# Kernel optimization log

Measured on AMD Instinct MI355X. Metric: run time of the kernel, lower is better.

Reference implementation:

```python
import jax, jax.numpy as jnp
import numpy as np
import math

STRIDE = ((2, 2), (4, 4), (8, 8), (16, 16))  # (ws, hs) pairs
D_MODEL = 256
B, H, W = 8, 128, 128
BN_EPS = 1e-5
LEAKY_SLOPE = 0.2


def setup_inputs() -> dict:
    key = jax.random.key(0)
    ks = jax.random.split(key, 8)
    s = 1.0 / math.sqrt(D_MODEL)
    s3 = 1.0 / math.sqrt(D_MODEL * 9)
    return {
        "x": jax.random.normal(ks[0], (B, D_MODEL, H, W), jnp.float32),
        "wq": jax.random.normal(ks[1], (D_MODEL, D_MODEL, 1, 1), jnp.float32) * s,
        "bq": jnp.zeros((D_MODEL,), jnp.float32),
        "wk": jax.random.normal(ks[2], (D_MODEL, D_MODEL, 1, 1), jnp.float32) * s,
        "bk": jnp.zeros((D_MODEL,), jnp.float32),
        "wv": jax.random.normal(ks[3], (D_MODEL, D_MODEL, 1, 1), jnp.float32) * s,
        "bv": jnp.zeros((D_MODEL,), jnp.float32),
        "wo": jax.random.normal(ks[4], (D_MODEL, D_MODEL, 3, 3), jnp.float32) * s3,
        "bo": jnp.zeros((D_MODEL,), jnp.float32),
        "gamma": jnp.ones((D_MODEL,), jnp.float32),
        "beta": jnp.zeros((D_MODEL,), jnp.float32),
    }


def _conv1x1(x, w, bias):
    # 1x1 conv == channel matmul
    return jnp.einsum('bchw,oc->bohw', x, w[:, :, 0, 0]) + bias[None, :, None, None]


def reference(x, wq, bq, wk, bk, wv, bv, wo, bo, gamma, beta):
    b, c, h, w = x.shape
    n = len(STRIDE)
    d_k = c // n
    q = _conv1x1(x, wq, bq)
    k = _conv1x1(x, wk, bk)
    v = _conv1x1(x, wv, bv)
    outs = []
    for idx, (ws, hs) in enumerate(STRIDE):
        lo = idx * d_k
        oh, ow = h // hs, w // ws

        def gather(t):
            # strided patch gather: element (i,j) head <- t[:, :, i::hs, j::ws]
            t = t[:, lo:lo + d_k].reshape(b, d_k, oh, hs, ow, ws)
            return t.transpose(0, 3, 5, 1, 2, 4).reshape(b, hs * ws, d_k * oh * ow)

        qi, ki, vi = gather(q), gather(k), gather(v)
        scale = 1.0 / jnp.sqrt(jnp.asarray(qi.shape[-1], qi.dtype))
        scores = jnp.einsum('bsd,btd->bst', qi, ki) * scale  # [b, hs*ws, hs*ws]
        p = jax.nn.softmax(scores, axis=-1)
        y = jnp.einsum('bst,btd->bsd', p, vi)
        # scatter back exactly as the torch permute(0,3,1,4,2,5): h = i*oh + row
        y = y.reshape(b, hs, ws, d_k, oh, ow).transpose(0, 3, 1, 4, 2, 5).reshape(b, d_k, h, w)
        outs.append(y)
    out = jnp.concatenate(outs, axis=1)  # [b, c, h, w]
    # output_linear: 3x3 conv -> BatchNorm2d (training-mode batch stats) -> LeakyReLU(0.2)
    out = jax.lax.conv_general_dilated(out, wo, (1, 1), 'SAME',
                                       dimension_numbers=('NCHW', 'OIHW', 'NCHW'))
    out = out + bo[None, :, None, None]
    mean = out.mean(axis=(0, 2, 3))
    var = out.var(axis=(0, 2, 3))
    out = (out - mean[None, :, None, None]) * jax.lax.rsqrt(var[None, :, None, None] + BN_EPS)
    out = out * gamma[None, :, None, None] + beta[None, :, None, None]
    return jnp.where(out > 0, out, LEAKY_SLOPE * out)
```

## Files before the change

kernel.cpp:

```cpp
#include <hip/hip_runtime.h>
#include <stdint.h>


#define DEVI static __device__ __forceinline__

typedef short bf8 __attribute__((ext_vector_type(8)));
typedef float f32x4 __attribute__((ext_vector_type(4)));

DEVI unsigned short f2bf(float f) {
  unsigned u = __builtin_bit_cast(unsigned, f);
  u = (u + 0x7fffu + ((u >> 16) & 1u)) >> 16;
  return (unsigned short)u;
}
DEVI float bf2f(unsigned short h) {
  unsigned u = ((unsigned)h) << 16;
  return __builtin_bit_cast(float, u);
}

DEVI void gload16(const void* g, void* l) {
  __builtin_amdgcn_global_load_lds(
      (const __attribute__((address_space(1))) unsigned int*)g,
      (__attribute__((address_space(3))) unsigned int*)l, 16, 0, 0);
}

static const size_t WB_OFF  = 0;
static const size_t WOB_OFF = 393216;
static const size_t QN_OFF  = 1572864;
static const size_t KN_OFF  = QN_OFF + 67108864;
static const size_t VN_OFF  = KN_OFF + 67108864;
static const size_t YN_OFF  = VN_OFF + 67108864;
static const size_t SC_OFF  = YN_OFF + 67108864;
static const size_t PRB_OFF = SC_OFF + 2236928;
static const size_t BNP_OFF = PRB_OFF + 1118464;
static const size_t BNS_OFF = BNP_OFF + 4194304;
static const size_t ZP_OFF  = BNS_OFF + 2048;
static const size_t WS_NEED = ZP_OFF + 256;

__global__ void k_prep(const float* __restrict__ wq, const float* __restrict__ wk,
                       const float* __restrict__ wv, const float* __restrict__ wo,
                       unsigned short* __restrict__ Wb, unsigned short* __restrict__ Wob) {
  int i = blockIdx.x * 256 + threadIdx.x;
  if (i < 196608) {
    int z = i >> 16, r = i & 65535;
    const float* w = (z == 0) ? wq : (z == 1) ? wk : wv;
    Wb[i] = f2bf(w[r]);
  } else {
    int j = i - 196608;
    int o = j / 2304, k = j - o * 2304;
    int e = k >> 8, c = k & 255;
    Wob[j] = f2bf(wo[(o * 256 + c) * 9 + e]);
  }
}

__global__ void k_zero(float* __restrict__ p, int n) {
  int i = blockIdx.x * 256 + threadIdx.x;
  for (; i < n; i += gridDim.x * 256) p[i] = 0.f;
}

__global__ __launch_bounds__(256, 3) void k_qkv(
    const float* __restrict__ x, const unsigned short* __restrict__ Wb,
    const float* __restrict__ bq, const float* __restrict__ bk, const float* __restrict__ bv,
    unsigned short* __restrict__ Qn, unsigned short* __restrict__ Kn,
    unsigned short* __restrict__ Vn) {
  const int pt = blockIdx.x, b = blockIdx.y;
  const int p0 = pt * 64;
  const int tid = threadIdx.x;

  __shared__ __align__(16) unsigned short xt[64 * 256];
  __shared__ __align__(16) unsigned short ot[32 * 256];

  const float* xb = x + (size_t)b * 256 * 16384;
  for (int k = 0; k < 16; ++k) {
    int i = tid + k * 256;
    int c = i >> 4, p4 = (i & 15) * 4;
    float4 v = *(const float4*)(xb + (size_t)c * 16384 + p0 + p4);
    xt[(p4 + 0) * 256 + (c ^ (((p4 + 0) & 7) << 3))] = f2bf(v.x);
    xt[(p4 + 1) * 256 + (c ^ (((p4 + 1) & 7) << 3))] = f2bf(v.y);
    xt[(p4 + 2) * 256 + (c ^ (((p4 + 2) & 7) << 3))] = f2bf(v.z);
    xt[(p4 + 3) * 256 + (c ^ (((p4 + 3) & 7) << 3))] = f2bf(v.w);
  }
  __syncthreads();

  const int wave = tid >> 6, lane = tid & 63;
  const int lr = lane & 15, lk = lane >> 4;
  const int obase = wave * 64;

  for (int z = 0; z < 3; ++z) {
    const unsigned short* Wz = Wb + (size_t)z * 65536;
    f32x4 acc[4][4];
    for (int m = 0; m < 4; ++m)
      for (int n = 0; n < 4; ++n)
        for (int r = 0; r < 4; ++r) acc[m][n][r] = 0.f;

    for (int ks = 0; ks < 8; ++ks) {
      int c0 = ks * 32 + lk * 8;
      bf8 a[4], bb[4];
#pragma unroll
      for (int m = 0; m < 4; ++m)
        a[m] = *(const bf8*)(Wz + (size_t)(obase + m * 16 + lr) * 256 + c0);
#pragma unroll
      for (int n = 0; n < 4; ++n) {
        int p = n * 16 + lr;
        bb[n] = *(const bf8*)(&xt[p * 256 + (c0 ^ ((p & 7) << 3))]);
      }
#pragma unroll
      for (int m = 0; m < 4; ++m)
#pragma unroll
        for (int n = 0; n < 4; ++n)
          acc[m][n] = __builtin_amdgcn_mfma_f32_16x16x32_bf16(a[m], bb[n], acc[m][n], 0, 0, 0);
    }

    const float* bias = (z == 0) ? bq : (z == 1) ? bk : bv;
    unsigned short* On = (z == 0) ? Qn : (z == 1) ? Kn : Vn;
    for (int h = 0; h < 2; ++h) {
      __syncthreads();
#pragma unroll
      for (int m = 0; m < 4; ++m) {
        int ob4 = obase + m * 16 + lk * 4;
        float4 b4 = *(const float4*)(bias + ob4);
#pragma unroll
        for (int nn = 0; nn < 2; ++nn) {
          int n = h * 2 + nn;
          int pch = nn * 16 + lr;
          ushort4 v4;
          v4.x = f2bf(acc[m][n][0] + b4.x);
          v4.y = f2bf(acc[m][n][1] + b4.y);
          v4.z = f2bf(acc[m][n][2] + b4.z);
          v4.w = f2bf(acc[m][n][3] + b4.w);
          *(ushort4*)(&ot[pch * 256 + (ob4 ^ ((pch & 7) << 3))]) = v4;
        }
      }
      __syncthreads();
      unsigned short* gb = On + ((size_t)b * 16384 + p0 + h * 32) * 256;
#pragma unroll
      for (int i = 0; i < 4; ++i) {
        int ch = tid + i * 256;
        *(uint4*)(gb + ch * 8) = *(const uint4*)(&ot[ch * 8]);
      }
    }
  }
}

template <int IDX>
__global__ __launch_bounds__(256) void k_gram(
    const unsigned short* __restrict__ Qn, const unsigned short* __restrict__ Kn,
    float* __restrict__ scores) {
  constexpr int HS = 2 << IDX, S = HS * HS, OH = 64 >> IDX, NSP = OH * OH;
  constexpr int SPW = (IDX == 2) ? 2 : 8;
  constexpr int DSUB = SPW * 64;
  constexpr int SPB = NSP / 32;
  constexpr int STEPS = SPB / SPW;
  constexpr int ROWS = S;
  constexpr int TPT = S * SPW * 8 / 256;
  constexpr int SCOFF = (IDX == 0) ? 0 : (IDX == 1) ? 128 : 2176;
  constexpr int HC = IDX * 64;
  constexpr int MT = (IDX == 2) ? 4 : 1;

  const int chk = blockIdx.x, b = blockIdx.y;
  const int tid = threadIdx.x;
  const int wave = tid >> 6, lane = tid & 63, lr = lane & 15, lk = lane >> 4;

  __shared__ __align__(16) unsigned short qg[ROWS * DSUB];
  __shared__ __align__(16) unsigned short kg[ROWS * DSUB];
  __shared__ float red[S * S];

  const size_t base = (size_t)b * 16384 * 256;

  f32x4 acc[MT][MT];
  for (int m = 0; m < MT; ++m)
    for (int n = 0; n < MT; ++n)
      for (int r = 0; r < 4; ++r) acc[m][n][r] = 0.f;

  for (int st = 0; st < STEPS; ++st) {
    const int sp0 = chk * SPB + st * SPW;
    __syncthreads();
#pragma unroll
    for (int r = 0; r < TPT; ++r) {
      int task = tid + r * 256;
      int cg = task & 7, pl = task >> 3;
      int spl = pl >> (2 * (IDX + 1)), s = pl & (S - 1);
      int sp = sp0 + spl;
      int ohi = sp >> (6 - IDX), owi = sp & (OH - 1);
      int ii = s >> (IDX + 1), jj = s & (HS - 1);
      int p = (ohi * HS + ii) * 128 + owi * HS + jj;
      size_t gaddr = base + (size_t)p * 256 + HC + ((cg ^ (p & 7)) << 3);
      int laddr = s * DSUB + (((spl * 8 + cg) ^ (s & 7)) << 3);
      *(uint4*)(qg + laddr) = *(const uint4*)(Qn + gaddr);
      *(uint4*)(kg + laddr) = *(const uint4*)(Kn + gaddr);
    }
    __syncthreads();
    if (IDX == 2) {
      int kgid = wave * 4 + lk;
      bf8 a[4], bb[4];
#pragma unroll
      for (int m = 0; m < 4; ++m) {
        int row = m * 16 + lr;
        int off = row * DSUB + ((kgid ^ (row & 7)) << 3);
        a[m] = *(const bf8*)(qg + off);
        bb[m] = *(const bf8*)(kg + off);
      }
#pragma unroll
      for (int m = 0; m < 4; ++m)
#pragma unroll
        for (int n = 0; n < 4; ++n)
          acc[m][n] = __builtin_amdgcn_mfma_f32_16x16x32_bf16(a[m], bb[n], acc[m][n], 0, 0, 0);
    } else {
      int row = lr & (ROWS - 1);
#pragma unroll
      for (int kk = 0; kk < 4; ++kk) {
        int kgid = (wave * 4 + kk) * 4 + lk;
        int off = row * DSUB + ((kgid ^ (row & 7)) << 3);
        bf8 a = *(const bf8*)(qg + off);
        bf8 bb = *(const bf8*)(kg + off);
        acc[0][0] = __builtin_amdgcn_mfma_f32_16x16x32_bf16(a, bb, acc[0][0], 0, 0, 0);
      }
    }
  }

  __syncthreads();
  for (int i2 = tid; i2 < S * S; i2 += 256) red[i2] = 0.f;
  __syncthreads();
  if (IDX == 2) {
#pragma unroll
    for (int m = 0; m < 4; ++m)
#pragma unroll
      for (int n = 0; n < 4; ++n)
#pragma unroll
        for (int r = 0; r < 4; ++r)
          atomicAdd(&red[(m * 16 + lk * 4 + r) * 64 + n * 16 + lr], acc[m][n][r]);
  } else if (IDX == 1) {
#pragma unroll
    for (int r = 0; r < 4; ++r)
      atomicAdd(&red[(lk * 4 + r) * 16 + lr], acc[0][0][r]);
  } else {
    if (lk == 0 && lr < 4) {
#pragma unroll
      for (int r = 0; r < 4; ++r)
        atomicAdd(&red[r * 4 + lr], acc[0][0][r]);
    }
  }
  __syncthreads();
  float* sc = scores + SCOFF + (size_t)b * S * S;
  for (int i2 = tid; i2 < S * S; i2 += 256) atomicAdd(sc + i2, red[i2]);
}

__global__ __launch_bounds__(256) void k_gram3(
    const unsigned short* __restrict__ Qn, const unsigned short* __restrict__ Kn,
    float* __restrict__ part3) {
  const int qc = blockIdx.x, tq = blockIdx.y, b = blockIdx.z;
  const int tid = threadIdx.x;
  const int wave = tid >> 6, lane = tid & 63, lr = lane & 15, lk = lane >> 4;

  __shared__ __align__(16) unsigned short qg[256 * 64];
  __shared__ __align__(16) unsigned short kg[64 * 64];

  const size_t base = (size_t)b * 16384 * 256;

  f32x4 acc[4][4];
  for (int m = 0; m < 4; ++m)
    for (int n = 0; n < 4; ++n)
      for (int r = 0; r < 4; ++r) acc[m][n][r] = 0.f;

  for (int st = 0; st < 8; ++st) {
    int sp = qc * 8 + st;
    int ohi = sp >> 3, owi = sp & 7;
    __syncthreads();
#pragma unroll
    for (int r = 0; r < 8; ++r) {
      int task = tid + r * 256;
      int cg = task & 7, s = task >> 3;
      int p = (ohi * 16 + (s >> 4)) * 128 + owi * 16 + (s & 15);
      uint4 v = *(const uint4*)(Qn + base + (size_t)p * 256 + 192 + ((cg ^ (p & 7)) << 3));
      *(uint4*)(qg + s * 64 + ((cg ^ (s & 7)) << 3)) = v;
    }
#pragma unroll
    for (int r = 0; r < 2; ++r) {
      int task = tid + r * 256;
      int cg = task & 7, tl = task >> 3;
      int p = (ohi * 16 + tq * 4 + (tl >> 4)) * 128 + owi * 16 + (tl & 15);
      uint4 v = *(const uint4*)(Kn + base + (size_t)p * 256 + 192 + ((cg ^ (p & 7)) << 3));
      *(uint4*)(kg + tl * 64 + ((cg ^ (tl & 7)) << 3)) = v;
    }
    __syncthreads();
#pragma unroll
    for (int kk = 0; kk < 2; ++kk) {
      int kgid = kk * 4 + lk;
      bf8 a[4], bb[4];
#pragma unroll
      for (int m = 0; m < 4; ++m) {
        int row = wave * 64 + m * 16 + lr;
        a[m] = *(const bf8*)(qg + row * 64 + ((kgid ^ (row & 7)) << 3));
      }
#pragma unroll
      for (int n = 0; n < 4; ++n) {
        int rowb = n * 16 + lr;
        bb[n] = *(const bf8*)(kg + rowb * 64 + ((kgid ^ (rowb & 7)) << 3));
      }
#pragma unroll
      for (int m = 0; m < 4; ++m)
#pragma unroll
        for (int n = 0; n < 4; ++n)
          acc[m][n] = __builtin_amdgcn_mfma_f32_16x16x32_bf16(a[m], bb[n], acc[m][n], 0, 0, 0);
    }
  }

  float* pb = part3 + (((size_t)qc * 8 + b) * 65536);
#pragma unroll
  for (int m = 0; m < 4; ++m)
#pragma unroll
    for (int r = 0; r < 4; ++r) {
      int srow = wave * 64 + m * 16 + lk * 4 + r;
#pragma unroll
      for (int n = 0; n < 4; ++n)
        pb[srow * 256 + tq * 64 + n * 16 + lr] = acc[m][n][r];
    }
}

__global__ __launch_bounds__(256) void k_softmax(const float* __restrict__ scores,
                                                 unsigned short* __restrict__ prb) {
  const int idx = blockIdx.x, b = blockIdx.y;
  const int S = 4 << (2 * idx);
  const int off = (idx == 0 ? 0 : idx == 1 ? 128 : 2176) + b * S * S;
  const int s = threadIdx.x;
  if (s >= S) return;
  const float scale = rsqrtf(64.0f * (float)(4096 >> (2 * idx)));
  const float* row = scores + off + s * S;
  float m = -1e30f;
  for (int t = 0; t < S; ++t) m = fmaxf(m, row[t]);
  m *= scale;
  float sum = 0.f;
  for (int t = 0; t < S; ++t) sum += __expf(row[t] * scale - m);
  float inv = 1.0f / sum;
  unsigned short* prow = prb + off + s * S;
  for (int t = 0; t < S; ++t) prow[t] = f2bf(__expf(row[t] * scale - m) * inv);
}

__global__ __launch_bounds__(256) void k_softmax3(const float* __restrict__ part3,
                                                  unsigned short* __restrict__ prb) {
  const int sc_ = blockIdx.x, b = blockIdx.y;
  const int tid = threadIdx.x;
  const int s = sc_ * 32 + (tid >> 3);
  const int t0 = (tid & 7) * 32;
  float v[32];
#pragma unroll
  for (int k = 0; k < 32; ++k) v[k] = 0.f;
  for (int q = 0; q < 8; ++q) {
    const float4* pp = (const float4*)(part3 + (((size_t)q * 8 + b) * 256 + s) * 256 + t0);
#pragma unroll
    for (int k = 0; k < 8; ++k) {
      float4 u = pp[k];
      v[k * 4 + 0] += u.x; v[k * 4 + 1] += u.y; v[k * 4 + 2] += u.z; v[k * 4 + 3] += u.w;
    }
  }
  const float scale = 1.0f / 64.0f;
  float m = -1e30f;
#pragma unroll
  for (int k = 0; k < 32; ++k) { v[k] *= scale; m = fmaxf(m, v[k]); }
  m = fmaxf(m, __shfl_xor(m, 1));
  m = fmaxf(m, __shfl_xor(m, 2));
  m = fmaxf(m, __shfl_xor(m, 4));
  float sum = 0.f;
#pragma unroll
  for (int k = 0; k < 32; ++k) { v[k] = __expf(v[k] - m); sum += v[k]; }
  sum += __shfl_xor(sum, 1);
  sum += __shfl_xor(sum, 2);
  sum += __shfl_xor(sum, 4);
  float inv = 1.0f / sum;
  unsigned short* prw = prb + 34944 + (size_t)b * 65536 + s * 256 + t0;
#pragma unroll
  for (int k8 = 0; k8 < 4; ++k8) {
    unsigned short tmp[8];
#pragma unroll
    for (int e = 0; e < 8; ++e) tmp[e] = f2bf(v[k8 * 8 + e] * inv);
    *(uint4*)(prw + k8 * 8) = *(const uint4*)tmp;
  }
}

template <int IDX>
__global__ __launch_bounds__(256) void k_pv(
    const unsigned short* __restrict__ Vn, const unsigned short* __restrict__ prb,
    unsigned short* __restrict__ Yn) {
  constexpr int HS = 2 << IDX, S = HS * HS, OH = 64 >> IDX;
  constexpr int IT = (IDX == 0) ? 8 : (IDX == 1) ? 4 : 1;
  constexpr int POFF = (IDX == 0) ? 0 : (IDX == 1) ? 128 : 2176;
  const int bx = blockIdx.x, b = blockIdx.y;
  const int c = threadIdx.x & 63, spg = threadIdx.x >> 6;
  __shared__ __align__(16) float pl[S * S];
  const unsigned short* pr = prb + POFF + (size_t)b * S * S;
  for (int i = threadIdx.x; i < S * S; i += 256) pl[i] = bf2f(pr[i]);
  __syncthreads();
  const int hc = IDX * 64;
  const unsigned short* vb = Vn + (size_t)b * 16384 * 256;
  unsigned short* yb = Yn + (size_t)b * 16384 * 256;
  for (int it = 0; it < IT; ++it) {
    int sp = bx * (4 * IT) + it * 4 + spg;
    int ohi = sp >> (6 - IDX), owi = sp & (OH - 1);
    float v[S];
#pragma unroll
    for (int t = 0; t < S; ++t) {
      int po = (ohi * HS + t / HS) * 128 + owi * HS + (t % HS);
      v[t] = bf2f(vb[(size_t)po * 256 + ((hc + c) ^ ((po & 7) << 3))]);
    }
    for (int s = 0; s < S; ++s) {
      const float4* p4 = (const float4*)(pl + s * S);
      float a = 0.f;
#pragma unroll
      for (int t4 = 0; t4 < S / 4; ++t4) {
        float4 pp = p4[t4];
        a += pp.x * v[t4 * 4] + pp.y * v[t4 * 4 + 1] + pp.z * v[t4 * 4 + 2] + pp.w * v[t4 * 4 + 3];
      }
      int po = ((s >> (IDX + 1)) * OH + ohi) * 128 + (s & (HS - 1)) * OH + owi;
      yb[(size_t)po * 256 + ((hc + c) ^ ((po & 7) << 3))] = f2bf(a);
    }
  }
}

__global__ __launch_bounds__(256) void k_pv3(
    const unsigned short* __restrict__ Vn, const unsigned short* __restrict__ prb,
    unsigned short* __restrict__ Yn) {
  const int sp = blockIdx.x, b = blockIdx.y;
  const int ohi = sp >> 3, owi = sp & 7;
  const int tid = threadIdx.x;
  __shared__ __align__(16) unsigned short vl[64 * 256];
  const unsigned short* vb = Vn + (size_t)b * 16384 * 256;
  {
    int t = tid;
    int po = (ohi * 16 + (t >> 4)) * 128 + owi * 16 + (t & 15);
    const unsigned short* src = vb + (size_t)po * 256;
    int xv = (po & 7) << 3;
#pragma unroll
    for (int g = 0; g < 8; ++g) {
      ushort4 lo = *(const ushort4*)(src + ((192 + g * 8) ^ xv));
      ushort4 hi = *(const ushort4*)(src + ((192 + g * 8) ^ xv) + 4);
      unsigned short vv[8] = {lo.x, lo.y, lo.z, lo.w, hi.x, hi.y, hi.z, hi.w};
#pragma unroll
      for (int e = 0; e < 8; ++e) {
        int cc = g * 8 + e;
        vl[cc * 256 + (t ^ ((cc & 7) << 3))] = vv[e];
      }
    }
  }
  __syncthreads();

  const int wave = tid >> 6, lane = tid & 63;
  const int lr = lane & 15, lk = lane >> 4;
  const int sb = wave * 64;
  const unsigned short* pr = prb + 34944 + (size_t)b * 65536;

  f32x4 acc[4][4];
  for (int m = 0; m < 4; ++m)
    for (int n = 0; n < 4; ++n)
      for (int r = 0; r < 4; ++r) acc[m][n][r] = 0.f;

  for (int kk = 0; kk < 8; ++kk) {
    int t0 = kk * 32 + lk * 8;
    bf8 a[4], bb[4];
#pragma unroll
    for (int m = 0; m < 4; ++m)
      a[m] = *(const bf8*)(pr + (size_t)(sb + m * 16 + lr) * 256 + t0);
#pragma unroll
    for (int n = 0; n < 4; ++n) {
      int cc = n * 16 + lr;
      bb[n] = *(const bf8*)(&vl[cc * 256 + (t0 ^ ((cc & 7) << 3))]);
    }
#pragma unroll
    for (int m = 0; m < 4; ++m)
#pragma unroll
      for (int n = 0; n < 4; ++n)
        acc[m][n] = __builtin_amdgcn_mfma_f32_16x16x32_bf16(a[m], bb[n], acc[m][n], 0, 0, 0);
  }

  unsigned short* yb = Yn + (size_t)b * 16384 * 256;
#pragma unroll
  for (int m = 0; m < 4; ++m) {
#pragma unroll
    for (int r = 0; r < 4; ++r) {
      int s = sb + m * 16 + lk * 4 + r;
      int si = s >> 4, sj = s & 15;
      int po = (si * 8 + ohi) * 128 + sj * 8 + owi;
#pragma unroll
      for (int n = 0; n < 4; ++n) {
        int cc = 192 + n * 16 + lr;
        yb[(size_t)po * 256 + (cc ^ (owi << 3))] = f2bf(acc[m][n][r]);
      }
    }
  }
}

#define CONV_PHASE(KT_, R_, PK_, DOSTAGE_, WAITMODE_)                            \
  do {                                                                           \
    if (DOSTAGE_) {                                                              \
      constexpr int type_ = (R_ == 0) ? 0 : (R_ == 1) ? 2 : (R_ == 2) ? 3 : 1;   \
      STAGE((1 - (PK_)) * 4 + (R_), type_, (KT_) + 1);                           \
    }                                                                            \
    if ((WAITMODE_) == 0) { asm volatile("s_waitcnt vmcnt(6)" ::: "memory"); }   \
    else if ((WAITMODE_) == 1) { asm volatile("s_waitcnt vmcnt(0)" ::: "memory"); } \
    __builtin_amdgcn_s_barrier();                                                \
    asm volatile("" ::: "memory");                                               \
    {                                                                            \
      constexpr int mh_ = (R_) >> 1, nh_ = (R_) & 1;                             \
      constexpr int sA_ = (PK_) * 4 + (mh_ ? 3 : 0);                             \
      constexpr int sB_ = (PK_) * 4 + (nh_ ? 2 : 1);                             \
      if (nh_ == 0) {                                                            \
        _Pragma("unroll") for (int m2 = 0; m2 < 4; ++m2) {                       \
          int row = wm * 64 + m2 * 16 + lr;                                      \
          _Pragma("unroll") for (int kk = 0; kk < 2; ++kk)                       \
            areg[m2][kk] = *(const bf8*)(&lds[sA_][row * 64 +                    \
                (((kk * 4 + lk) ^ (row & 7)) << 3)]);                            \
        }                                                                        \
      }                                                                          \
      bf8 breg[2][2];                                                            \
      _Pragma("unroll") for (int n2 = 0; n2 < 2; ++n2) {                         \
        int row = wn * 32 + n2 * 16 + lr;                                        \
        _Pragma("unroll") for (int kk = 0; kk < 2; ++kk)                         \
          breg[n2][kk] = *(const bf8*)(&lds[sB_][row * 64 +                      \
              (((kk * 4 + lk) ^ (row & 7)) << 3)]);                              \
      }                                                                          \
      __builtin_amdgcn_s_setprio(1);                                             \
      _Pragma("unroll") for (int kk = 0; kk < 2; ++kk)                           \
        _Pragma("unroll") for (int m2 = 0; m2 < 4; ++m2)                         \
          _Pragma("unroll") for (int n2 = 0; n2 < 2; ++n2)                       \
            acc[mh_ * 4 + m2][nh_ * 2 + n2] =                                    \
                __builtin_amdgcn_mfma_f32_16x16x32_bf16(                         \
                    areg[m2][kk], breg[n2][kk],                                  \
                    acc[mh_ * 4 + m2][nh_ * 2 + n2], 0, 0, 0);                   \
      __builtin_amdgcn_s_setprio(0);                                             \
      asm volatile("" ::: "memory");                                             \
    }                                                                            \
  } while (0)

__global__ __launch_bounds__(512, 2) void k_conv(
    const unsigned short* __restrict__ Yn, const unsigned short* __restrict__ Wob,
    const float* __restrict__ bo, const unsigned short* __restrict__ zp,
    unsigned short* __restrict__ co, float* __restrict__ bnp) {
  __shared__ __align__(16) unsigned short lds[8][8192];

  const int bid = blockIdx.x;
  const int swz = (bid & 7) * 64 + (bid >> 3);
  const int b = swz >> 6, tile = swz & 63;
  const int y0 = (tile >> 3) * 16, x0 = (tile & 7) * 16;
  const int tid = threadIdx.x;
  const int wave = tid >> 6, lane = tid & 63;
  const int lr = lane & 15, lk = lane >> 4;
  const int wm = wave >> 2, wn = wave & 3;
  const int cg = lane & 7;

  const unsigned short* yb = Yn + (size_t)b * 16384 * 256;

  auto STAGE = [&](int slot, int type, int KT) {
    if (type < 2) {
      const unsigned short* wsrc = Wob + (KT >> 2) * 256 + (KT & 3) * 64;
#pragma unroll
      for (int j = 0; j < 2; ++j) {
        int rp = (wave * 2 + j) * 8 + (lane >> 3);
        int o = ((rp >> 6) & 1) * 128 + type * 64 + (rp & 63);
        int kg = cg ^ (rp & 7);
        gload16(wsrc + o * 2304 + (kg << 3), &lds[slot][(wave * 2 + j) * 512]);
      }
    } else {
      int e = KT >> 2;
      int dy = e / 3 - 1, dx = e % 3 - 1, c8 = (KT & 3) * 8;
#pragma unroll
      for (int j = 0; j < 2; ++j) {
        int rp = (wave * 2 + j) * 8 + (lane >> 3);
        int n = ((rp >> 5) & 3) * 64 + (type - 2) * 32 + (rp & 31);
        int kg = cg ^ (rp & 7);
        int h = y0 + (n >> 4) + dy, ww = x0 + (n & 15) + dx;
        const unsigned short* src = zp;
        if (h >= 0 && h < 128 && ww >= 0 && ww < 128) {
          int pp = h * 128 + ww;
          src = yb + (size_t)pp * 256 + ((c8 + (kg ^ (pp & 7))) << 3);
        }
        gload16(src, &lds[slot][(wave * 2 + j) * 512]);
      }
    }
  };

  f32x4 acc[8][4];
#pragma unroll
  for (int m = 0; m < 8; ++m)
#pragma unroll
    for (int n = 0; n < 4; ++n)
#pragma unroll
      for (int r = 0; r < 4; ++r) acc[m][n][r] = 0.f;

  bf8 areg[4][2];

  STAGE(0, 0, 0); STAGE(1, 2, 0); STAGE(2, 3, 0); STAGE(3, 1, 0);
  asm volatile("s_waitcnt vmcnt(0)" ::: "memory");

  for (int gg = 0; gg < 17; ++gg) {
    const int k0 = gg * 2;
    CONV_PHASE(k0, 0, 0, true, 0);
    CONV_PHASE(k0, 1, 0, true, 0);
    CONV_PHASE(k0, 2, 0, true, 0);
    CONV_PHASE(k0, 3, 0, true, 0);
    CONV_PHASE(k0 + 1, 0, 1, true, 0);
    CONV_PHASE(k0 + 1, 1, 1, true, 0);
    CONV_PHASE(k0 + 1, 2, 1, true, 0);
    CONV_PHASE(k0 + 1, 3, 1, true, 0);
  }
  CONV_PHASE(34, 0, 0, true, 0);
  CONV_PHASE(34, 1, 0, true, 0);
  CONV_PHASE(34, 2, 0, true, 0);
  CONV_PHASE(34, 3, 0, true, 0);
  CONV_PHASE(35, 0, 1, false, 1);
  CONV_PHASE(35, 1, 1, false, 2);
  CONV_PHASE(35, 2, 1, false, 2);
  CONV_PHASE(35, 3, 1, false, 2);

  __syncthreads();
  unsigned short* cb = co + (size_t)b * 256 * 16384;
  float* red1 = (float*)&lds[0][0];
  float* red2 = red1 + 1024;
#pragma unroll
  for (int m = 0; m < 8; ++m) {
#pragma unroll
    for (int r = 0; r < 4; ++r) {
      int o = wm * 128 + m * 16 + lk * 4 + r;
      float bvv = bo[o];
      float s1 = 0.f, s2 = 0.f;
#pragma unroll
      for (int n = 0; n < 4; ++n) {
        int pix = wn * 64 + n * 16 + lr;
        int py = pix >> 4, px = pix & 15;
        float v = acc[m][n][r] + bvv;
        cb[(size_t)o * 16384 + (y0 + py) * 128 + x0 + px] = f2bf(v);
        s1 += v;
        s2 += v * v;
      }
      for (int off = 1; off < 16; off <<= 1) {
        s1 += __shfl_xor(s1, off, 64);
        s2 += __shfl_xor(s2, off, 64);
      }
      if (lr == 0) {
        int ol = m * 16 + lk * 4 + r;
        red1[wave * 128 + ol] = s1;
        red2[wave * 128 + ol] = s2;
      }
    }
  }
  __syncthreads();
  {
    int o = tid & 255, stat = tid >> 8;
    int wm2 = o >> 7, ol = o & 127;
    const float* rd = stat ? red2 : red1;
    float s = rd[(wm2 * 4 + 0) * 128 + ol] + rd[(wm2 * 4 + 1) * 128 + ol] +
              rd[(wm2 * 4 + 2) * 128 + ol] + rd[(wm2 * 4 + 3) * 128 + ol];
    bnp[((size_t)(b * 64 + tile) * 256 + o) * 2 + stat] = s;
  }
}

__global__ __launch_bounds__(256) void k_bnred(
    const float* __restrict__ bnp, const float* __restrict__ gamma,
    const float* __restrict__ beta, float* __restrict__ bns) {
  const int o = blockIdx.x;
  const int tid = threadIdx.x;
  float s1 = 0.f, s2 = 0.f;
  for (int k = tid; k < 512; k += 256) {
    s1 += bnp[((size_t)k * 256 + o) * 2 + 0];
    s2 += bnp[((size_t)k * 256 + o) * 2 + 1];
  }
  __shared__ float r1[256], r2[256];
  r1[tid] = s1; r2[tid] = s2;
  __syncthreads();
  for (int off = 128; off > 0; off >>= 1) {
    if (tid < off) { r1[tid] += r1[tid + off]; r2[tid] += r2[tid + off]; }
    __syncthreads();
  }
  if (tid == 0) {
    const float cnt = 8.0f * 16384.0f;
    float mean = r1[0] / cnt;
    float var = r2[0] / cnt - mean * mean;
    float sc = gamma[o] * rsqrtf(var + 1e-5f);
    bns[o] = sc;
    bns[256 + o] = beta[o] - mean * sc;
  }
}

__global__ void k_bnapply(const unsigned short* __restrict__ co, float* __restrict__ out,
                          const float* __restrict__ bns) {
  size_t i = ((size_t)blockIdx.x * 256 + threadIdx.x) * 8;
  const size_t total = 33554432;
  const size_t stride = (size_t)gridDim.x * 256 * 8;
  for (; i < total; i += stride) {
    uint4 v = *(const uint4*)(co + i);
    int o = (int)((i >> 14) & 255);
    float sc = bns[o], shv = bns[256 + o];
    const unsigned short* pv = (const unsigned short*)&v;
    float r[8];
#pragma unroll
    for (int e = 0; e < 8; ++e) {
      float f = bf2f(pv[e]) * sc + shv;
      r[e] = f > 0.f ? f : 0.2f * f;
    }
    *(float4*)(out + i) = *(const float4*)&r[0];
    *(float4*)(out + i + 4) = *(const float4*)&r[4];
  }
}

extern "C" void kernel_launch(void* const* d_in, const int* in_sizes, int n_in,
                              void* d_out, int out_size, void* d_ws, size_t ws_size,
                              hipStream_t stream) {
  if (ws_size < WS_NEED) return;

  const float* x     = (const float*)d_in[0];
  const float* wq    = (const float*)d_in[1];
  const float* bq    = (const float*)d_in[2];
  const float* wk    = (const float*)d_in[3];
  const float* bk    = (const float*)d_in[4];
  const float* wv    = (const float*)d_in[5];
  const float* bv    = (const float*)d_in[6];
  const float* wo    = (const float*)d_in[7];
  const float* bo    = (const float*)d_in[8];
  const float* gamma = (const float*)d_in[9];
  const float* beta  = (const float*)d_in[10];
  float* out = (float*)d_out;
  char* ws = (char*)d_ws;

  unsigned short* Wb  = (unsigned short*)(ws + WB_OFF);
  unsigned short* Wob = (unsigned short*)(ws + WOB_OFF);
  unsigned short* Qn  = (unsigned short*)(ws + QN_OFF);
  unsigned short* Kn  = (unsigned short*)(ws + KN_OFF);
  unsigned short* Vn  = (unsigned short*)(ws + VN_OFF);
  unsigned short* Yn  = (unsigned short*)(ws + YN_OFF);
  float* part3 = (float*)(ws + YN_OFF);
  unsigned short* co = (unsigned short*)(ws + QN_OFF);
  float* scores = (float*)(ws + SC_OFF);
  unsigned short* prb = (unsigned short*)(ws + PRB_OFF);
  float* bnp    = (float*)(ws + BNP_OFF);
  float* bns    = (float*)(ws + BNS_OFF);
  unsigned short* zp = (unsigned short*)(ws + ZP_OFF);

  k_prep<<<dim3(3072), dim3(256), 0, stream>>>(wq, wk, wv, wo, Wb, Wob);
  k_zero<<<dim3(137), dim3(256), 0, stream>>>(scores, 34944);
  k_zero<<<dim3(1), dim3(64), 0, stream>>>((float*)zp, 64);
  k_qkv<<<dim3(256, 8), dim3(256), 0, stream>>>(x, Wb, bq, bk, bv, Qn, Kn, Vn);
  k_gram<0><<<dim3(32, 8), dim3(256), 0, stream>>>(Qn, Kn, scores);
  k_gram<1><<<dim3(32, 8), dim3(256), 0, stream>>>(Qn, Kn, scores);
  k_gram<2><<<dim3(32, 8), dim3(256), 0, stream>>>(Qn, Kn, scores);
  k_gram3<<<dim3(8, 4, 8), dim3(256), 0, stream>>>(Qn, Kn, part3);
  k_softmax<<<dim3(3, 8), dim3(256), 0, stream>>>(scores, prb);
  k_softmax3<<<dim3(8, 8), dim3(256), 0, stream>>>(part3, prb);
  k_pv<0><<<dim3(128, 8), dim3(256), 0, stream>>>(Vn, prb, Yn);
  k_pv<1><<<dim3(64, 8), dim3(256), 0, stream>>>(Vn, prb, Yn);
  k_pv<2><<<dim3(64, 8), dim3(256), 0, stream>>>(Vn, prb, Yn);
  k_pv3<<<dim3(64, 8), dim3(256), 0, stream>>>(Vn, prb, Yn);
  k_conv<<<dim3(512), dim3(512), 0, stream>>>(Yn, Wob, bo, zp, co, bnp);
  k_bnred<<<dim3(256), dim3(256), 0, stream>>>(bnp, gamma, beta, bns);
  k_bnapply<<<dim3(4096), dim3(256), 0, stream>>>(co, out, bns);
}
```

Before: 572.0 us.

## Hoist conv staging address math, reuse B fragments, merge zero kernels

The 3x3 conv main loop now runs over the 9 kernel taps with quarter-phase unrolling. Per-thread load offsets are precomputed once, so each stage does only cheap adds and one bounds check instead of divides and mods. B-operand fragments are loaded only in the first two phases of each quarter and reused for the second M half, which cuts LDS reads. The two zeroing kernels are merged into one launch, and the qkv MFMA block gets raised wave priority. The cost is more live VGPRs for breg and the precomputed offsets, which could reduce occupancy or cause spills.

```diff
diff --git a/kernel.cpp b/kernel.cpp
--- a/kernel.cpp
+++ b/kernel.cpp
@@ -52,9 +52,11 @@
   }
 }
 
-__global__ void k_zero(float* __restrict__ p, int n) {
+__global__ void k_zero2(float* __restrict__ a, int na, float* __restrict__ b2, int nb) {
   int i = blockIdx.x * 256 + threadIdx.x;
-  for (; i < n; i += gridDim.x * 256) p[i] = 0.f;
+  for (; i < na + nb; i += gridDim.x * 256) {
+    if (i < na) a[i] = 0.f; else b2[i - na] = 0.f;
+  }
 }
 
 __global__ __launch_bounds__(256, 3) void k_qkv(
@@ -103,11 +105,13 @@
         int p = n * 16 + lr;
         bb[n] = *(const bf8*)(&xt[p * 256 + (c0 ^ ((p & 7) << 3))]);
       }
+      __builtin_amdgcn_s_setprio(1);
 #pragma unroll
       for (int m = 0; m < 4; ++m)
 #pragma unroll
         for (int n = 0; n < 4; ++n)
           acc[m][n] = __builtin_amdgcn_mfma_f32_16x16x32_bf16(a[m], bb[n], acc[m][n], 0, 0, 0);
+      __builtin_amdgcn_s_setprio(0);
     }
 
     const float* bias = (z == 0) ? bq : (z == 1) ? bk : bv;
@@ -487,21 +491,28 @@
   }
 }
 
-#define CONV_PHASE(KT_, R_, PK_, DOSTAGE_, WAITMODE_)                            \
+#define CPHASE(Q_, R_, DOSTAGE_, WM_)                                            \
   do {                                                                           \
+    constexpr int PK_ = (Q_) & 1;                                                \
     if (DOSTAGE_) {                                                              \
-      constexpr int type_ = (R_ == 0) ? 0 : (R_ == 1) ? 2 : (R_ == 2) ? 3 : 1;   \
-      STAGE((1 - (PK_)) * 4 + (R_), type_, (KT_) + 1);                           \
+      constexpr int QN_ = ((Q_) + 1) & 3;                                        \
+      constexpr bool NE_ = ((Q_) == 3);                                          \
+      const int sdy = NE_ ? dyN : dy, sdx = NE_ ? dxN : dx;                      \
+      const int se = NE_ ? (e + 1) : e;                                          \
+      constexpr int slot_ = (1 - PK_) * 4 + (R_);                                \
+      if ((R_) == 0) STAGE_A(slot_, 0, se, QN_);                                 \
+      else if ((R_) == 1) STAGE_B(slot_, 0, sdy, sdx, QN_);                      \
+      else if ((R_) == 2) STAGE_B(slot_, 1, sdy, sdx, QN_);                      \
+      else STAGE_A(slot_, 1, se, QN_);                                           \
     }                                                                            \
-    if ((WAITMODE_) == 0) { asm volatile("s_waitcnt vmcnt(6)" ::: "memory"); }   \
-    else if ((WAITMODE_) == 1) { asm volatile("s_waitcnt vmcnt(0)" ::: "memory"); } \
+    if ((WM_) == 0) { asm volatile("s_waitcnt vmcnt(6)" ::: "memory"); }         \
+    else if ((WM_) == 1) { asm volatile("s_waitcnt vmcnt(0)" ::: "memory"); }    \
     __builtin_amdgcn_s_barrier();                                                \
     asm volatile("" ::: "memory");                                               \
     {                                                                            \
       constexpr int mh_ = (R_) >> 1, nh_ = (R_) & 1;                             \
-      constexpr int sA_ = (PK_) * 4 + (mh_ ? 3 : 0);                             \
-      constexpr int sB_ = (PK_) * 4 + (nh_ ? 2 : 1);                             \
       if (nh_ == 0) {                                                            \
+        constexpr int sA_ = PK_ * 4 + (mh_ ? 3 : 0);                             \
         _Pragma("unroll") for (int m2 = 0; m2 < 4; ++m2) {                       \
           int row = wm * 64 + m2 * 16 + lr;                                      \
           _Pragma("unroll") for (int kk = 0; kk < 2; ++kk)                       \
@@ -509,12 +520,14 @@
                 (((kk * 4 + lk) ^ (row & 7)) << 3)]);                            \
         }                                                                        \
       }                                                                          \
-      bf8 breg[2][2];                                                            \
-      _Pragma("unroll") for (int n2 = 0; n2 < 2; ++n2) {                         \
-        int row = wn * 32 + n2 * 16 + lr;                                        \
-        _Pragma("unroll") for (int kk = 0; kk < 2; ++kk)                         \
-          breg[n2][kk] = *(const bf8*)(&lds[sB_][row * 64 +                      \
-              (((kk * 4 + lk) ^ (row & 7)) << 3)]);                              \
+      if ((R_) < 2) {                                                            \
+        constexpr int sB_ = PK_ * 4 + ((R_) ? 2 : 1);                            \
+        _Pragma("unroll") for (int n2 = 0; n2 < 2; ++n2) {                       \
+          int row = wn * 32 + n2 * 16 + lr;                                      \
+          _Pragma("unroll") for (int kk = 0; kk < 2; ++kk)                       \
+            breg[R_][n2][kk] = *(const bf8*)(&lds[sB_][row * 64 +                \
+                (((kk * 4 + lk) ^ (row & 7)) << 3)]);                            \
+        }                                                                        \
       }                                                                          \
       __builtin_amdgcn_s_setprio(1);                                             \
       _Pragma("unroll") for (int kk = 0; kk < 2; ++kk)                           \
@@ -522,7 +535,7 @@
           _Pragma("unroll") for (int n2 = 0; n2 < 2; ++n2)                       \
             acc[mh_ * 4 + m2][nh_ * 2 + n2] =                                    \
                 __builtin_amdgcn_mfma_f32_16x16x32_bf16(                         \
-                    areg[m2][kk], breg[n2][kk],                                  \
+                    areg[m2][kk], breg[nh_][n2][kk],                             \
                     acc[mh_ * 4 + m2][nh_ * 2 + n2], 0, 0, 0);                   \
       __builtin_amdgcn_s_setprio(0);                                             \
       asm volatile("" ::: "memory");                                             \
@@ -547,34 +560,41 @@
 
   const unsigned short* yb = Yn + (size_t)b * 16384 * 256;
 
-  auto STAGE = [&](int slot, int type, int KT) {
-    if (type < 2) {
-      const unsigned short* wsrc = Wob + (KT >> 2) * 256 + (KT & 3) * 64;
-#pragma unroll
-      for (int j = 0; j < 2; ++j) {
-        int rp = (wave * 2 + j) * 8 + (lane >> 3);
-        int o = ((rp >> 6) & 1) * 128 + type * 64 + (rp & 63);
-        int kg = cg ^ (rp & 7);
-        gload16(wsrc + o * 2304 + (kg << 3), &lds[slot][(wave * 2 + j) * 512]);
-      }
-    } else {
-      int e = KT >> 2;
-      int dy = e / 3 - 1, dx = e % 3 - 1, c8 = (KT & 3) * 8;
-#pragma unroll
-      for (int j = 0; j < 2; ++j) {
-        int rp = (wave * 2 + j) * 8 + (lane >> 3);
-        int n = ((rp >> 5) & 3) * 64 + (type - 2) * 32 + (rp & 31);
-        int kg = cg ^ (rp & 7);
-        int h = y0 + (n >> 4) + dy, ww = x0 + (n & 15) + dx;
-        const unsigned short* src = zp;
-        if (h >= 0 && h < 128 && ww >= 0 && ww < 128) {
-          int pp = h * 128 + ww;
-          src = yb + (size_t)pp * 256 + ((c8 + (kg ^ (pp & 7))) << 3);
-        }
-        gload16(src, &lds[slot][(wave * 2 + j) * 512]);
-      }
-    }
+  const int rp0 = wave * 16 + (lane >> 3), rp1 = rp0 + 8;
+  const int kg0 = cg ^ (rp0 & 7), kg1 = cg ^ (rp1 & 7);
+  const int aoffA0 = ((rp0 >> 6) * 128 + (rp0 & 63)) * 2304 + kg0 * 8;
+  const int aoffA1 = ((rp1 >> 6) * 128 + (rp1 & 63)) * 2304 + kg1 * 8;
+  const int n00 = ((rp0 >> 5) & 3) * 64 + (rp0 & 31);
+  const int n01 = ((rp1 >> 5) & 3) * 64 + (rp1 & 31);
+  const int hB0 = y0 + (n00 >> 4), wB0 = x0 + (n00 & 15);
+  const int hB1 = y0 + (n01 >> 4), wB1 = x0 + (n01 & 15);
+  const int ppB0 = hB0 * 128 + wB0, ppB1 = hB1 * 128 + wB1;
+  const int ld0 = (wave * 2 + 0) * 512, ld1 = (wave * 2 + 1) * 512;
+
+  auto STAGE_A = [&](int slot, int T, int eS, int qS) {
+    const unsigned short* basep = Wob + eS * 256 + qS * 64 + T * 147456;
+    gload16(basep + aoffA0, &lds[slot][ld0]);
+    gload16(basep + aoffA1, &lds[slot][ld1]);
   };
+  auto STAGE_B = [&](int slot, int T3, int dyS, int dxS, int qS) {
+    const int so = dyS * 128 + dxS + T3 * 256;
+    const int hS = dyS + T3 * 2;
+    const int q8 = qS * 8;
+    {
+      int pp = ppB0 + so;
+      int h = hB0 + hS, w = wB0 + dxS;
+      const unsigned short* s1 = yb + (ptrdiff_t)pp * 256 + ((q8 + (kg0 ^ (pp & 7))) << 3);
+      const unsigned short* src = ((unsigned)h < 128u && (unsigned)w < 128u) ? s1 : zp;
+      gload16(src, &lds[slot][ld0]);
+    }
+    {
+      int pp = ppB1 + so;
+      int h = hB1 + hS, w = wB1 + dxS;
+      const unsigned short* s1 = yb + (ptrdiff_t)pp * 256 + ((q8 + (kg1 ^ (pp & 7))) << 3);
+      const unsigned short* src = ((unsigned)h < 128u && (unsigned)w < 128u) ? s1 : zp;
+      gload16(src, &lds[slot][ld1]);
+    }
+  };
 
   f32x4 acc[8][4];
 #pragma unroll
@@ -585,29 +605,29 @@
       for (int r = 0; r < 4; ++r) acc[m][n][r] = 0.f;
 
   bf8 areg[4][2];
-
-  STAGE(0, 0, 0); STAGE(1, 2, 0); STAGE(2, 3, 0); STAGE(3, 1, 0);
+  bf8 breg[2][2][2];
+
+  STAGE_A(0, 0, 0, 0); STAGE_B(1, 0, -1, -1, 0); STAGE_B(2, 1, -1, -1, 0); STAGE_A(3, 1, 0, 0);
   asm volatile("s_waitcnt vmcnt(0)" ::: "memory");
 
-  for (int gg = 0; gg < 17; ++gg) {
-    const int k0 = gg * 2;
-    CONV_PHASE(k0, 0, 0, true, 0);
-    CONV_PHASE(k0, 1, 0, true, 0);
-    CONV_PHASE(k0, 2, 0, true, 0);
-    CONV_PHASE(k0, 3, 0, true, 0);
-    CONV_PHASE(k0 + 1, 0, 1, true, 0);
-    CONV_PHASE(k0 + 1, 1, 1, true, 0);
-    CONV_PHASE(k0 + 1, 2, 1, true, 0);
-    CONV_PHASE(k0 + 1, 3, 1, true, 0);
-  }
-  CONV_PHASE(34, 0, 0, true, 0);
-  CONV_PHASE(34, 1, 0, true, 0);
-  CONV_PHASE(34, 2, 0, true, 0);
-  CONV_PHASE(34, 3, 0, true, 0);
-  CONV_PHASE(35, 0, 1, false, 1);
-  CONV_PHASE(35, 1, 1, false, 2);
-  CONV_PHASE(35, 2, 1, false, 2);
-  CONV_PHASE(35, 3, 1, false, 2);
+  int dy = -1, dx = -1;
+  for (int e = 0; e < 8; ++e) {
+    int dyN = ((e + 1) >= 6) ? 1 : (((e + 1) >= 3) ? 0 : -1);
+    int dxN = (e + 1) - (dyN + 1) * 3 - 1;
+    CPHASE(0, 0, true, 0); CPHASE(0, 1, true, 0); CPHASE(0, 2, true, 0); CPHASE(0, 3, true, 0);
+    CPHASE(1, 0, true, 0); CPHASE(1, 1, true, 0); CPHASE(1, 2, true, 0); CPHASE(1, 3, true, 0);
+    CPHASE(2, 0, true, 0); CPHASE(2, 1, true, 0); CPHASE(2, 2, true, 0); CPHASE(2, 3, true, 0);
+    CPHASE(3, 0, true, 0); CPHASE(3, 1, true, 0); CPHASE(3, 2, true, 0); CPHASE(3, 3, true, 0);
+    dy = dyN; dx = dxN;
+  }
+  {
+    const int e = 8;
+    const int dyN = 1, dxN = 1;
+    CPHASE(0, 0, true, 0); CPHASE(0, 1, true, 0); CPHASE(0, 2, true, 0); CPHASE(0, 3, true, 0);
+    CPHASE(1, 0, true, 0); CPHASE(1, 1, true, 0); CPHASE(1, 2, true, 0); CPHASE(1, 3, true, 0);
+    CPHASE(2, 0, true, 0); CPHASE(2, 1, true, 0); CPHASE(2, 2, true, 0); CPHASE(2, 3, true, 0);
+    CPHASE(3, 0, false, 1); CPHASE(3, 1, false, 2); CPHASE(3, 2, false, 2); CPHASE(3, 3, false, 2);
+  }
 
   __syncthreads();
   unsigned short* cb = co + (size_t)b * 256 * 16384;
@@ -733,8 +753,7 @@
   unsigned short* zp = (unsigned short*)(ws + ZP_OFF);
 
   k_prep<<<dim3(3072), dim3(256), 0, stream>>>(wq, wk, wv, wo, Wb, Wob);
-  k_zero<<<dim3(137), dim3(256), 0, stream>>>(scores, 34944);
-  k_zero<<<dim3(1), dim3(64), 0, stream>>>((float*)zp, 64);
+  k_zero2<<<dim3(137), dim3(256), 0, stream>>>(scores, 34944, (float*)zp, 64);
   k_qkv<<<dim3(256, 8), dim3(256), 0, stream>>>(x, Wb, bq, bk, bv, Qn, Kn, Vn);
   k_gram<0><<<dim3(32, 8), dim3(256), 0, stream>>>(Qn, Kn, scores);
   k_gram<1><<<dim3(32, 8), dim3(256), 0, stream>>>(Qn, Kn, scores);
```

After: 729.4 us. 27.5% more time.
